# Optimization experiments

Hardware: AMD Instinct MI355X
Metric: run time of the kernel (lower is better)

The kernel has to match this reference:

```python
import jax, jax.numpy as jnp
import numpy as np

EMBED_DIM = 1024
NUM_HEADS = 16
HEAD_DIM = EMBED_DIM // NUM_HEADS
SCALE = HEAD_DIM ** -0.5


def setup_inputs() -> dict:
    key = jax.random.key(0)
    ks = jax.random.split(key, 9)
    B, S, D = 4, 2048, EMBED_DIM
    w_std = 1.0 / np.sqrt(D)
    x = jax.random.normal(ks[0], (B, S, D), dtype=jnp.float32)
    Wq = jax.random.uniform(ks[1], (D, D), jnp.float32, -w_std, w_std)
    bq = jax.random.uniform(ks[2], (D,), jnp.float32, -w_std, w_std)
    Wk = jax.random.uniform(ks[3], (D, D), jnp.float32, -w_std, w_std)
    bk = jax.random.uniform(ks[4], (D,), jnp.float32, -w_std, w_std)
    Wv = jax.random.uniform(ks[5], (D, D), jnp.float32, -w_std, w_std)
    bv = jax.random.uniform(ks[6], (D,), jnp.float32, -w_std, w_std)
    Wo = jax.random.uniform(ks[7], (D, D), jnp.float32, -w_std, w_std)
    bo = jax.random.uniform(ks[8], (D,), jnp.float32, -w_std, w_std)
    return {"x": x, "Wq": Wq, "bq": bq, "Wk": Wk, "bk": bk,
            "Wv": Wv, "bv": bv, "Wo": Wo, "bo": bo}


def reference(x, Wq, bq, Wk, bk, Wv, bv, Wo, bo):
    B, S, D = x.shape
    H, Dh = NUM_HEADS, HEAD_DIM
    # projections; Linear stores weight as [out,in] -> y = x @ W.T + b,
    # here W is stored as [D, D] used as x @ W + b (equivalent param'zation)
    q = (x @ Wq + bq).reshape(B, S, H, Dh).transpose(0, 2, 1, 3)  # [B,H,S,Dh]
    k = (x @ Wk + bk).reshape(B, S, H, Dh).transpose(0, 2, 1, 3)
    v = (x @ Wv + bv).reshape(B, S, H, Dh).transpose(0, 2, 1, 3)
    scores = jnp.einsum("bhqd,bhkd->bhqk", q, k) * SCALE  # [B,H,S,S]
    attn = jax.nn.softmax(scores, axis=-1)  # dropout is identity in eval mode
    out = jnp.einsum("bhqk,bhkd->bhqd", attn, v)  # [B,H,S,Dh]
    out = out.transpose(0, 2, 1, 3).reshape(B, S, D)
    return out @ Wo + bo
```

## Files before the change

kernel.cpp:

```cpp
#include <hip/hip_runtime.h>
#include <stdint.h>
#include <stddef.h>


typedef __attribute__((ext_vector_type(8)))  short          s16x8;
typedef __attribute__((ext_vector_type(8)))  unsigned short u16x8;
typedef __attribute__((ext_vector_type(4)))  unsigned short u16x4;
typedef __attribute__((ext_vector_type(4)))  float          f32x4;
typedef __attribute__((ext_vector_type(16))) float          f32x16;

#define DMODEL 1024
#define SEQ    2048
#define NHEAD  16
#define DHEAD  64
#define NTOK   8192
#define QSCALE 0.1803368801111244f

#define MFMA_B16(a, b, c) __builtin_amdgcn_mfma_f32_16x16x32_bf16((a), (b), (c), 0, 0, 0)
#define MFMA32(a, b, c)   __builtin_amdgcn_mfma_f32_32x32x16_bf16((a), (b), (c), 0, 0, 0)

__device__ __forceinline__ float bf2f(unsigned short u) {
  union { unsigned int i; float f; } v; v.i = ((unsigned int)u) << 16; return v.f;
}
__device__ __forceinline__ unsigned short f2bf(float f) {
  union { float f; unsigned int i; } v; v.f = f;
  unsigned int r = v.i + 0x7FFFu + ((v.i >> 16) & 1u);
  return (unsigned short)(r >> 16);
}
__device__ __forceinline__ float fexp2(float x) {
#if __has_builtin(__builtin_amdgcn_exp2f)
  return __builtin_amdgcn_exp2f(x);
#else
  return exp2f(x);
#endif
}
__device__ __forceinline__ unsigned int cvtpk(float a, float b) {
  unsigned int r;
  asm("v_cvt_pk_bf16_f32 %0, %1, %2" : "=v"(r) : "v"(a), "v"(b));
  return r;
}

__device__ __forceinline__ void gld16(const unsigned short* g, unsigned short* l) {
  __builtin_amdgcn_global_load_lds(
      (const __attribute__((address_space(1))) void*)g,
      (__attribute__((address_space(3))) void*)l, 16, 0, 0);
}
__device__ __forceinline__ void vmdrain() {
  asm volatile("s_waitcnt vmcnt(0)" ::: "memory");
}

__global__ void detect_fp32(const unsigned short* __restrict__ w, int* __restrict__ flag) {
  __shared__ int cnt;
  if (threadIdx.x == 0) cnt = 0;
  __syncthreads();
  int local = 0;
  for (int i = threadIdx.x; i < 8192; i += 256) {
    const unsigned short v = w[i];
    if ((v & 0x7F80u) >= 0x3F80u) local++;
  }
  atomicAdd(&cnt, local);
  __syncthreads();
  if (threadIdx.x == 0) *flag = (cnt >= 128) ? 1 : 0;
}

__global__ void norm_vec4(const void* __restrict__ s0, const void* __restrict__ s1,
                          const void* __restrict__ s2, const void* __restrict__ s3,
                          unsigned short* __restrict__ d0, unsigned short* __restrict__ d1,
                          unsigned short* __restrict__ d2, unsigned short* __restrict__ d3,
                          const int* __restrict__ flag) {
  const int fl = *flag;
  const int v = blockIdx.y;
  const void* src = (v == 0) ? s0 : (v == 1) ? s1 : (v == 2) ? s2 : s3;
  unsigned short* dst = (v == 0) ? d0 : (v == 1) ? d1 : (v == 2) ? d2 : d3;
  const int i = blockIdx.x * 256 + threadIdx.x;
  dst[i] = fl ? f2bf(((const float*)src)[i]) : ((const unsigned short*)src)[i];
}

__global__ __launch_bounds__(256) void norm_x(const void* __restrict__ src,
                                              unsigned short* __restrict__ dst,
                                              const int* __restrict__ flag) {
  const int fl = *flag;
  const size_t i = ((size_t)blockIdx.x * 256 + threadIdx.x) * 8;
  if (fl) {
    const float* s = (const float*)src + i;
    u16x8 o;
#pragma unroll
    for (int j = 0; j < 8; ++j) o[j] = f2bf(s[j]);
    *(u16x8*)(dst + i) = o;
  } else {
    *(u16x8*)(dst + i) = *(const u16x8*)((const unsigned short*)src + i);
  }
}

__global__ __launch_bounds__(256) void transpose4(const void* __restrict__ i0,
                                                  const void* __restrict__ i1,
                                                  const void* __restrict__ i2,
                                                  const void* __restrict__ i3,
                                                  unsigned short* __restrict__ o0,
                                                  unsigned short* __restrict__ o1,
                                                  unsigned short* __restrict__ o2,
                                                  unsigned short* __restrict__ o3,
                                                  const int* __restrict__ flag) {
  __shared__ unsigned short tile[64][65];
  const int z = blockIdx.z;
  const void* in = (z == 0) ? i0 : (z == 1) ? i1 : (z == 2) ? i2 : i3;
  unsigned short* out = (z == 0) ? o0 : (z == 1) ? o1 : (z == 2) ? o2 : o3;
  const int fl = *flag;
  const int tx = threadIdx.x;
  const int ty = threadIdx.y;
  const int bx = blockIdx.x * 64;
  const int by = blockIdx.y * 64;
  const float* inf = (const float*)in;
  const unsigned short* inu = (const unsigned short*)in;
#pragma unroll
  for (int i = 0; i < 16; ++i) {
    const int r = i * 4 + ty;
    const size_t idx = (size_t)(by + r) * DMODEL + bx + tx;
    tile[r][tx] = fl ? f2bf(inf[idx]) : inu[idx];
  }
  __syncthreads();
#pragma unroll
  for (int i = 0; i < 16; ++i) {
    const int r = i * 4 + ty;
    out[(size_t)(bx + r) * DMODEL + by + tx] = tile[tx][r];
  }
}

template <int MODE>
__global__ __launch_bounds__(256) void gemm_bt(const unsigned short* __restrict__ A,
                                               const unsigned short* __restrict__ Bt,
                                               const unsigned short* __restrict__ bias0,
                                               const unsigned short* __restrict__ bias1,
                                               unsigned short* __restrict__ C0,
                                               unsigned short* __restrict__ C1,
                                               float* __restrict__ Cf) {
  __shared__ __align__(16) unsigned short As[2 * 128 * 32];
  __shared__ __align__(16) unsigned short Bs[2 * 128 * 32];

  const int t = threadIdx.x;
  const int wv = t >> 6;
  const int lane = t & 63;
  const int q4 = lane >> 4;
  const int c  = lane & 15;
  const int wm = wv >> 1;
  const int wn = wv & 1;
  const int m0 = blockIdx.x * 128;
  const int n0 = blockIdx.y * 128;

  f32x4 acc[4][4];
#pragma unroll
  for (int i = 0; i < 4; ++i)
#pragma unroll
    for (int j = 0; j < 4; ++j) acc[i][j] = (f32x4){0.f, 0.f, 0.f, 0.f};

  const int ch0 = wv * 128 + lane;
  const int ch1 = ch0 + 64;
  const unsigned short* Ag0 = A  + (size_t)(m0 + (ch0 >> 2)) * DMODEL + (ch0 & 3) * 8;
  const unsigned short* Ag1 = A  + (size_t)(m0 + (ch1 >> 2)) * DMODEL + (ch1 & 3) * 8;
  const unsigned short* Bg0 = Bt + (size_t)(n0 + (ch0 >> 2)) * DMODEL + (ch0 & 3) * 8;
  const unsigned short* Bg1 = Bt + (size_t)(n0 + (ch1 >> 2)) * DMODEL + (ch1 & 3) * 8;
  const int lb0 = (wv * 2 + 0) * 512;
  const int lb1 = (wv * 2 + 1) * 512;

  gld16(Ag0, As + lb0);
  gld16(Ag1, As + lb1);
  gld16(Bg0, Bs + lb0);
  gld16(Bg1, Bs + lb1);

  for (int k0 = 0; k0 < DMODEL; k0 += 32) {
    const int cur = (k0 >> 5) & 1;
    vmdrain();
    __syncthreads();
    if (k0 + 32 < DMODEL) {
      unsigned short* Ab = As + (cur ^ 1) * 4096;
      unsigned short* Bb = Bs + (cur ^ 1) * 4096;
      gld16(Ag0 + k0 + 32, Ab + lb0);
      gld16(Ag1 + k0 + 32, Ab + lb1);
      gld16(Bg0 + k0 + 32, Bb + lb0);
      gld16(Bg1 + k0 + 32, Bb + lb1);
    }
    const unsigned short* Ac = As + cur * 4096;
    const unsigned short* Bc = Bs + cur * 4096;

    s16x8 af[4], bfr[4];
#pragma unroll
    for (int i = 0; i < 4; ++i)
      af[i] = *(const s16x8*)(Ac + (wm * 64 + i * 16 + c) * 32 + q4 * 8);
#pragma unroll
    for (int j = 0; j < 4; ++j)
      bfr[j] = *(const s16x8*)(Bc + (wn * 64 + j * 16 + c) * 32 + q4 * 8);
    __builtin_amdgcn_s_setprio(1);
#pragma unroll
    for (int i = 0; i < 4; ++i)
#pragma unroll
      for (int j = 0; j < 4; ++j) acc[i][j] = MFMA_B16(af[i], bfr[j], acc[i][j]);
    __builtin_amdgcn_s_setprio(0);
  }

  if (MODE == 2) {
#pragma unroll
    for (int i = 0; i < 4; ++i) {
#pragma unroll
      for (int rg = 0; rg < 4; ++rg) {
        const int m = m0 + wm * 64 + i * 16 + q4 * 4 + rg;
        const float bval = bf2f(bias0[m]);
#pragma unroll
        for (int j = 0; j < 4; ++j) {
          const int n = n0 + wn * 64 + j * 16 + c;
          C0[(((size_t)(n >> 11) * 1024 + m) << 11) + (n & 2047)] =
              f2bf(acc[i][j][rg] + bval);
        }
      }
    }
  } else {
#pragma unroll
    for (int j = 0; j < 4; ++j) {
      const int n = n0 + wn * 64 + j * 16 + c;
      float bval;
      if (MODE == 0) {
        bval = bf2f(bias0[n]);
      } else {
        bval = bf2f((n < 1024) ? bias0[n] : bias1[n & 1023]);
      }
#pragma unroll
      for (int i = 0; i < 4; ++i) {
#pragma unroll
        for (int rg = 0; rg < 4; ++rg) {
          const int m = m0 + wm * 64 + i * 16 + q4 * 4 + rg;
          const float oval = acc[i][j][rg] + bval;
          if (MODE == 0) {
            Cf[(size_t)m * DMODEL + n] = oval;
          } else {
            const int d = n & 1023;
            const int h = d >> 6, dh = d & 63;
            const int b = m >> 11, s = m & 2047;
            const size_t idx = ((((size_t)b * NHEAD + h) * SEQ + s) << 6) + dh;
            if (n < 1024) C0[idx] = f2bf(oval * QSCALE);
            else          C1[idx] = f2bf(oval);
          }
        }
      }
    }
  }
}

__global__ void copyout(const float* __restrict__ X, void* __restrict__ out,
                        const int* __restrict__ flag) {
  const int fl = *flag;
  const size_t i = (size_t)blockIdx.x * 1024 + threadIdx.x * 4;
#pragma unroll
  for (int j = 0; j < 4; ++j) {
    const float v = X[i + j];
    if (fl) ((float*)out)[i + j] = v;
    else    ((unsigned short*)out)[i + j] = f2bf(v);
  }
}

__global__ __launch_bounds__(256, 2) void attn_fused(const unsigned short* __restrict__ Qg,
                                                     const unsigned short* __restrict__ Kg,
                                                     const unsigned short* __restrict__ VTg,
                                                     unsigned short* __restrict__ Of) {
  __shared__ __align__(16) unsigned short smem[16384];

  const int t = threadIdx.x;
  const int wv = t >> 6;
  const int lane = t & 63;
  const int hi = lane >> 5;
  const int ql = lane & 31;
  const int bh = blockIdx.x;
  const int q0 = blockIdx.y * 256;
  const int b = bh >> 4, h = bh & 15;

  const unsigned short* Qb  = Qg  + ((size_t)bh * SEQ + q0 + wv * 64) * DHEAD;
  const unsigned short* Kb  = Kg  + (size_t)bh * SEQ * DHEAD;
  const unsigned short* VTb = VTg + (size_t)bh * DHEAD * SEQ;

  int koff[2], voff[2];
#pragma unroll
  for (int cl = 0; cl < 2; ++cl) {
    const int p = wv * 128 + cl * 64 + lane;
    const int row = p >> 3;
    const int slot = (p & 7) ^ (row & 7);
    koff[cl] = row * 64 + slot * 8;
    voff[cl] = row * 2048 + slot * 8;
  }
  int off[4];
#pragma unroll
  for (int s = 0; s < 4; ++s) off[s] = (((s * 2 + hi) ^ (ql & 7)) * 8);

  {
    unsigned short* Kd = smem;
    unsigned short* Vd = smem + 4096;
#pragma unroll
    for (int cl = 0; cl < 2; ++cl) {
      gld16(Kb + koff[cl], Kd + (wv * 128 + cl * 64) * 8);
      gld16(VTb + voff[cl], Vd + (wv * 128 + cl * 64) * 8);
    }
  }

  s16x8 qf[2][4];
#pragma unroll
  for (int qt = 0; qt < 2; ++qt)
#pragma unroll
    for (int s = 0; s < 4; ++s)
      qf[qt][s] = *(const s16x8*)(Qb + (size_t)(qt * 32 + ql) * DHEAD + s * 16 + hi * 8);

  f32x16 acco[2][2];
#pragma unroll
  for (int qt = 0; qt < 2; ++qt)
#pragma unroll
    for (int dt = 0; dt < 2; ++dt)
#pragma unroll
      for (int r = 0; r < 16; ++r) acco[qt][dt][r] = 0.f;
  f32x16 zv;
#pragma unroll
  for (int r = 0; r < 16; ++r) zv[r] = 0.f;
  float rs[2][4] = {{0.f, 0.f, 0.f, 0.f}, {0.f, 0.f, 0.f, 0.f}};

  for (int kt = 0; kt < SEQ / 64; ++kt) {
    vmdrain();
    __syncthreads();
    const int cur = kt & 1;
    if (kt + 1 < SEQ / 64) {
      unsigned short* Kd = smem + (cur ^ 1) * 8192;
      unsigned short* Vd = smem + (cur ^ 1) * 8192 + 4096;
      const unsigned short* Ksrc = Kb + (size_t)(kt + 1) * 64 * DHEAD;
      const unsigned short* Vsrc = VTb + (size_t)(kt + 1) * 64;
#pragma unroll
      for (int cl = 0; cl < 2; ++cl) {
        gld16(Ksrc + koff[cl], Kd + (wv * 128 + cl * 64) * 8);
        gld16(Vsrc + voff[cl], Vd + (wv * 128 + cl * 64) * 8);
      }
    }
    const unsigned short* Ksb = smem + cur * 8192;
    const unsigned short* Vtb = smem + cur * 8192 + 4096;

    f32x16 accs[2][2];
    __builtin_amdgcn_s_setprio(1);
#pragma unroll
    for (int k2 = 0; k2 < 2; ++k2) {
#pragma unroll
      for (int s = 0; s < 4; ++s) {
        const s16x8 kf = *(const s16x8*)(Ksb + (k2 * 32 + ql) * 64 + off[s]);
        if (s == 0) {
          accs[0][k2] = MFMA32(kf, qf[0][s], zv);
          accs[1][k2] = MFMA32(kf, qf[1][s], zv);
        } else {
          accs[0][k2] = MFMA32(kf, qf[0][s], accs[0][k2]);
          accs[1][k2] = MFMA32(kf, qf[1][s], accs[1][k2]);
        }
      }
    }
    __builtin_amdgcn_s_setprio(0);

    unsigned int u[2][2][8];
#pragma unroll
    for (int qt = 0; qt < 2; ++qt) {
#pragma unroll
      for (int k2 = 0; k2 < 2; ++k2) {
#pragma unroll
        for (int r = 0; r < 16; ++r) {
          const float p = fexp2(accs[qt][k2][r]);
          accs[qt][k2][r] = p;
          rs[qt][r & 3] += p;
        }
#pragma unroll
        for (int i = 0; i < 8; ++i)
          u[qt][k2][i] = cvtpk(accs[qt][k2][2 * i], accs[qt][k2][2 * i + 1]);
      }
    }

    __builtin_amdgcn_s_setprio(1);
#pragma unroll
    for (int k2 = 0; k2 < 2; ++k2) {
#pragma unroll
      for (int s = 0; s < 2; ++s) {
        const int kap = k2 * 2 + s;
        const s16x8 vf0 = *(const s16x8*)(Vtb + (0 * 32 + ql) * 64 + off[kap]);
        const s16x8 vf1 = *(const s16x8*)(Vtb + (1 * 32 + ql) * 64 + off[kap]);
#pragma unroll
        for (int qt = 0; qt < 2; ++qt) {
          unsigned int a0 = u[qt][k2][4 * s + 0], b0 = u[qt][k2][4 * s + 2];
          unsigned int a1 = u[qt][k2][4 * s + 1], b1 = u[qt][k2][4 * s + 3];
          asm("v_permlane32_swap_b32 %0, %1" : "+v"(a0), "+v"(b0));
          asm("v_permlane32_swap_b32 %0, %1" : "+v"(a1), "+v"(b1));
          union { unsigned int w[4]; s16x8 v; } pb;
          pb.w[0] = a0; pb.w[1] = a1; pb.w[2] = b0; pb.w[3] = b1;
          acco[qt][0] = MFMA32(vf0, pb.v, acco[qt][0]);
          acco[qt][1] = MFMA32(vf1, pb.v, acco[qt][1]);
        }
      }
    }
    __builtin_amdgcn_s_setprio(0);
  }

#pragma unroll
  for (int qt = 0; qt < 2; ++qt) {
    float lsum = (rs[qt][0] + rs[qt][1]) + (rs[qt][2] + rs[qt][3]);
    lsum += __shfl_xor(lsum, 32);
    const float inv = 1.0f / lsum;
    const int tok = q0 + wv * 64 + qt * 32 + ql;
    unsigned short* orow = Of + ((size_t)b * SEQ + tok) * DMODEL + h * DHEAD;
#pragma unroll
    for (int dt = 0; dt < 2; ++dt) {
#pragma unroll
      for (int rq = 0; rq < 4; ++rq) {
        u16x4 o;
#pragma unroll
        for (int j = 0; j < 4; ++j) o[j] = f2bf(acco[qt][dt][rq * 4 + j] * inv);
        *(u16x4*)(orow + dt * 32 + rq * 8 + hi * 4) = o;
      }
    }
  }
}

extern "C" void kernel_launch(void* const* d_in, const int* in_sizes, int n_in,
                              void* d_out, int out_size, void* d_ws, size_t ws_size,
                              hipStream_t stream) {
  const void* x  = d_in[0];
  const void* Wq = d_in[1];
  const void* bq = d_in[2];
  const void* Wk = d_in[3];
  const void* bk = d_in[4];
  const void* Wv = d_in[5];
  const void* bv = d_in[6];
  const void* Wo = d_in[7];
  const void* bo = d_in[8];

  unsigned short* ws = (unsigned short*)d_ws;
  const size_t M1 = (size_t)DMODEL * DMODEL;
  const size_t MQ = (size_t)NTOK * DMODEL;

  unsigned short* Qw  = ws;
  unsigned short* Kw  = Qw + MQ;
  unsigned short* Vw  = Kw + MQ;
  unsigned short* WqT = Vw + MQ;
  unsigned short* WkT = WqT + M1;
  unsigned short* WvT = WkT + M1;
  unsigned short* WoT = WvT + M1;
  unsigned short* bqn = WoT + M1;
  unsigned short* bkn = bqn + 1024;
  unsigned short* bvn = bkn + 1024;
  unsigned short* bon = bvn + 1024;
  int*            flg = (int*)(bon + 1024);
  float*          X   = (float*)Kw;
  unsigned short* Xb  = (unsigned short*)d_out;
  unsigned short* Ob  = (unsigned short*)d_out;

  detect_fp32<<<1, 256, 0, stream>>>((const unsigned short*)Wq, flg);

  norm_vec4<<<dim3(4, 4), 256, 0, stream>>>(bq, bk, bv, bo,
                                            bqn, bkn, bvn, bon, flg);

  transpose4<<<dim3(16, 16, 4), dim3(64, 4), 0, stream>>>(
      Wq, Wk, Wv, Wo, WqT, WkT, WvT, WoT, flg);

  norm_x<<<4096, 256, 0, stream>>>(x, Xb, flg);

  gemm_bt<1><<<dim3(64, 16), 256, 0, stream>>>(Xb, WqT, bqn, bkn, Qw, Kw, nullptr);
  gemm_bt<2><<<dim3(8, 64), 256, 0, stream>>>(WvT, Xb, bvn, nullptr, Vw, nullptr, nullptr);

  attn_fused<<<dim3(64, 8), 256, 0, stream>>>(Qw, Kw, Vw, Ob);

  gemm_bt<0><<<dim3(64, 8), 256, 0, stream>>>(Ob, WoT, bon, nullptr,
                                              nullptr, nullptr, X);
  copyout<<<8192, 256, 0, stream>>>(X, d_out, flg);
}
```

Before: 305.0 us.

## Fuse output dtype conversion into out-projection GEMM and write attention in-place

The out-projection GEMM now writes directly to the final output buffer in fp32 or bf16 based on the runtime flag, which removes the fp32 scratch buffer and the separate copyout kernel. Attention writes its output in head-major layout over the Q buffer in place, and the out-projection GEMM gathers its A operand from that [B,H,S,64] layout. This saves one kernel launch and a full fp32 round-trip through memory. The in-place overwrite of Q relies on each block reading only its own Q rows before writing them back.

```diff
diff --git a/kernel.cpp b/kernel.cpp
--- a/kernel.cpp
+++ b/kernel.cpp
@@ -133,7 +133,8 @@
                                                const unsigned short* __restrict__ bias1,
                                                unsigned short* __restrict__ C0,
                                                unsigned short* __restrict__ C1,
-                                               float* __restrict__ Cf) {
+                                               void* __restrict__ Cout,
+                                               const int* __restrict__ flag) {
   __shared__ __align__(16) unsigned short As[2 * 128 * 32];
   __shared__ __align__(16) unsigned short Bs[2 * 128 * 32];
 
@@ -155,15 +156,26 @@
 
   const int ch0 = wv * 128 + lane;
   const int ch1 = ch0 + 64;
-  const unsigned short* Ag0 = A  + (size_t)(m0 + (ch0 >> 2)) * DMODEL + (ch0 & 3) * 8;
-  const unsigned short* Ag1 = A  + (size_t)(m0 + (ch1 >> 2)) * DMODEL + (ch1 & 3) * 8;
-  const unsigned short* Bg0 = Bt + (size_t)(n0 + (ch0 >> 2)) * DMODEL + (ch0 & 3) * 8;
-  const unsigned short* Bg1 = Bt + (size_t)(n0 + (ch1 >> 2)) * DMODEL + (ch1 & 3) * 8;
+  const int ar0 = ch0 >> 2, ak0 = (ch0 & 3) * 8;
+  const int ar1 = ch1 >> 2, ak1 = (ch1 & 3) * 8;
+
+  auto aAddr = [&](int ar, int ak, int kk) -> const unsigned short* {
+    if constexpr (MODE == 0) {
+      const int m = m0 + ar;
+      const int kc = kk + ak;
+      return A + ((size_t)((m >> 11) * NHEAD + (kc >> 6)) * SEQ + (m & 2047)) * 64 +
+             (kc & 63);
+    } else {
+      return A + (size_t)(m0 + ar) * DMODEL + ak + kk;
+    }
+  };
+  const unsigned short* Bg0 = Bt + (size_t)(n0 + ar0) * DMODEL + ak0;
+  const unsigned short* Bg1 = Bt + (size_t)(n0 + ar1) * DMODEL + ak1;
   const int lb0 = (wv * 2 + 0) * 512;
   const int lb1 = (wv * 2 + 1) * 512;
 
-  gld16(Ag0, As + lb0);
-  gld16(Ag1, As + lb1);
+  gld16(aAddr(ar0, ak0, 0), As + lb0);
+  gld16(aAddr(ar1, ak1, 0), As + lb1);
   gld16(Bg0, Bs + lb0);
   gld16(Bg1, Bs + lb1);
 
@@ -174,8 +186,8 @@
     if (k0 + 32 < DMODEL) {
       unsigned short* Ab = As + (cur ^ 1) * 4096;
       unsigned short* Bb = Bs + (cur ^ 1) * 4096;
-      gld16(Ag0 + k0 + 32, Ab + lb0);
-      gld16(Ag1 + k0 + 32, Ab + lb1);
+      gld16(aAddr(ar0, ak0, k0 + 32), Ab + lb0);
+      gld16(aAddr(ar1, ak1, k0 + 32), Ab + lb1);
       gld16(Bg0 + k0 + 32, Bb + lb0);
       gld16(Bg1 + k0 + 32, Bb + lb1);
     }
@@ -212,54 +224,50 @@
         }
       }
     }
-  } else {
+  } else if (MODE == 0) {
+    const int fl = *flag;
 #pragma unroll
     for (int j = 0; j < 4; ++j) {
       const int n = n0 + wn * 64 + j * 16 + c;
-      float bval;
-      if (MODE == 0) {
-        bval = bf2f(bias0[n]);
-      } else {
-        bval = bf2f((n < 1024) ? bias0[n] : bias1[n & 1023]);
-      }
+      const float bval = bf2f(bias0[n]);
 #pragma unroll
       for (int i = 0; i < 4; ++i) {
 #pragma unroll
         for (int rg = 0; rg < 4; ++rg) {
           const int m = m0 + wm * 64 + i * 16 + q4 * 4 + rg;
           const float oval = acc[i][j][rg] + bval;
-          if (MODE == 0) {
-            Cf[(size_t)m * DMODEL + n] = oval;
-          } else {
-            const int d = n & 1023;
-            const int h = d >> 6, dh = d & 63;
-            const int b = m >> 11, s = m & 2047;
-            const size_t idx = ((((size_t)b * NHEAD + h) * SEQ + s) << 6) + dh;
-            if (n < 1024) C0[idx] = f2bf(oval * QSCALE);
-            else          C1[idx] = f2bf(oval);
-          }
-        }
-      }
-    }
-  }
-}
-
-__global__ void copyout(const float* __restrict__ X, void* __restrict__ out,
-                        const int* __restrict__ flag) {
-  const int fl = *flag;
-  const size_t i = (size_t)blockIdx.x * 1024 + threadIdx.x * 4;
-#pragma unroll
-  for (int j = 0; j < 4; ++j) {
-    const float v = X[i + j];
-    if (fl) ((float*)out)[i + j] = v;
-    else    ((unsigned short*)out)[i + j] = f2bf(v);
-  }
-}
-
-__global__ __launch_bounds__(256, 2) void attn_fused(const unsigned short* __restrict__ Qg,
+          if (fl) ((float*)Cout)[(size_t)m * DMODEL + n] = oval;
+          else    ((unsigned short*)Cout)[(size_t)m * DMODEL + n] = f2bf(oval);
+        }
+      }
+    }
+  } else {
+#pragma unroll
+    for (int j = 0; j < 4; ++j) {
+      const int n = n0 + wn * 64 + j * 16 + c;
+      const float bval = bf2f((n < 1024) ? bias0[n] : bias1[n & 1023]);
+#pragma unroll
+      for (int i = 0; i < 4; ++i) {
+#pragma unroll
+        for (int rg = 0; rg < 4; ++rg) {
+          const int m = m0 + wm * 64 + i * 16 + q4 * 4 + rg;
+          const float oval = acc[i][j][rg] + bval;
+          const int d = n & 1023;
+          const int h = d >> 6, dh = d & 63;
+          const int b = m >> 11, s = m & 2047;
+          const size_t idx = ((((size_t)b * NHEAD + h) * SEQ + s) << 6) + dh;
+          if (n < 1024) C0[idx] = f2bf(oval * QSCALE);
+          else          C1[idx] = f2bf(oval);
+        }
+      }
+    }
+  }
+}
+
+__global__ __launch_bounds__(256, 2) void attn_fused(const unsigned short* Qg,
                                                      const unsigned short* __restrict__ Kg,
                                                      const unsigned short* __restrict__ VTg,
-                                                     unsigned short* __restrict__ Of) {
+                                                     unsigned short* Oq) {
   __shared__ __align__(16) unsigned short smem[16384];
 
   const int t = threadIdx.x;
@@ -269,7 +277,6 @@
   const int ql = lane & 31;
   const int bh = blockIdx.x;
   const int q0 = blockIdx.y * 256;
-  const int b = bh >> 4, h = bh & 15;
 
   const unsigned short* Qb  = Qg  + ((size_t)bh * SEQ + q0 + wv * 64) * DHEAD;
   const unsigned short* Kb  = Kg  + (size_t)bh * SEQ * DHEAD;
@@ -400,7 +407,7 @@
     lsum += __shfl_xor(lsum, 32);
     const float inv = 1.0f / lsum;
     const int tok = q0 + wv * 64 + qt * 32 + ql;
-    unsigned short* orow = Of + ((size_t)b * SEQ + tok) * DMODEL + h * DHEAD;
+    unsigned short* orow = Oq + ((size_t)bh * SEQ + tok) * DHEAD;
 #pragma unroll
     for (int dt = 0; dt < 2; ++dt) {
 #pragma unroll
@@ -443,9 +450,7 @@
   unsigned short* bvn = bkn + 1024;
   unsigned short* bon = bvn + 1024;
   int*            flg = (int*)(bon + 1024);
-  float*          X   = (float*)Kw;
   unsigned short* Xb  = (unsigned short*)d_out;
-  unsigned short* Ob  = (unsigned short*)d_out;
 
   detect_fp32<<<1, 256, 0, stream>>>((const unsigned short*)Wq, flg);
 
@@ -457,12 +462,13 @@
 
   norm_x<<<4096, 256, 0, stream>>>(x, Xb, flg);
 
-  gemm_bt<1><<<dim3(64, 16), 256, 0, stream>>>(Xb, WqT, bqn, bkn, Qw, Kw, nullptr);
-  gemm_bt<2><<<dim3(8, 64), 256, 0, stream>>>(WvT, Xb, bvn, nullptr, Vw, nullptr, nullptr);
-
-  attn_fused<<<dim3(64, 8), 256, 0, stream>>>(Qw, Kw, Vw, Ob);
-
-  gemm_bt<0><<<dim3(64, 8), 256, 0, stream>>>(Ob, WoT, bon, nullptr,
-                                              nullptr, nullptr, X);
-  copyout<<<8192, 256, 0, stream>>>(X, d_out, flg);
-}
+  gemm_bt<1><<<dim3(64, 16), 256, 0, stream>>>(Xb, WqT, bqn, bkn, Qw, Kw,
+                                               nullptr, nullptr);
+  gemm_bt<2><<<dim3(8, 64), 256, 0, stream>>>(WvT, Xb, bvn, nullptr, Vw, nullptr,
+                                              nullptr, nullptr);
+
+  attn_fused<<<dim3(64, 8), 256, 0, stream>>>(Qw, Kw, Vw, Qw);
+
+  gemm_bt<0><<<dim3(64, 8), 256, 0, stream>>>(Qw, WoT, bon, nullptr,
+                                              nullptr, nullptr, d_out, flg);
+}
```

After: 288.7 us. 5.3% less time.
